# Kernel tuning notes

Measured on AMD Instinct MI355X. Metric: run time of the kernel, lower is better.

The kernel has to match this reference:

```python
import jax, jax.numpy as jnp
import numpy as np

D_K = 64
MASK_FILL = -1e9


def setup_inputs() -> dict:
    key = jax.random.key(0)
    kq, kk, kv, km = jax.random.split(key, 4)
    B, H, S, D = 2, 16, 2048, D_K
    q = jax.random.normal(kq, (B, H, S, D), dtype=jnp.float32)
    k = jax.random.normal(kk, (B, H, D, S), dtype=jnp.float32)  # pre-transposed keys
    v = jax.random.normal(kv, (B, H, S, D), dtype=jnp.float32)
    mask = jax.random.randint(km, (B, H, S, S), 0, 2).astype(jnp.bool_)
    return {"q": q, "k": k, "v": v, "mask": mask}


def reference(q, k, v, mask):
    # scores: [B, H, S, S] = q @ k (k already [B,H,D,S])
    scores = jnp.einsum("bhsd,bhdt->bhst", q, k) / jnp.sqrt(jnp.float32(D_K))
    scores = jnp.where(mask, MASK_FILL, scores)
    attn = jax.nn.softmax(scores, axis=-1)
    context = jnp.einsum("bhst,bhtd->bhsd", attn, v)
    return (context, attn)
```

## Files before the change

kernel.cpp:

```cpp
#include <hip/hip_runtime.h>

#define S_LEN    2048
#define DK       64
#define N_BH     32
#define ROWS     16
#define NTHREADS 512
#define ELDSW    2048

typedef float          f32x4  __attribute__((ext_vector_type(4)));
typedef int            i32x4  __attribute__((ext_vector_type(4)));
typedef short          bf16x8 __attribute__((ext_vector_type(8)));
typedef unsigned short u16x8  __attribute__((ext_vector_type(8)));

__device__ __forceinline__ unsigned short f2bf(float f) {
    unsigned u = __builtin_bit_cast(unsigned, f);
    u += 0x7fffu + ((u >> 16) & 1u);
    return (unsigned short)(u >> 16);
}
__device__ __forceinline__ float bf2f(unsigned short h) {
    unsigned u = ((unsigned)h) << 16;
    return __builtin_bit_cast(float, u);
}

__global__ void prep_qcast(const float* __restrict__ q, unsigned short* __restrict__ Qb) {
    const long i = ((long)blockIdx.x * 256 + threadIdx.x) * 8;
    f32x4 a = *(const f32x4*)(q + i);
    f32x4 b = *(const f32x4*)(q + i + 4);
    u16x8 o;
    o[0]=f2bf(a.x); o[1]=f2bf(a.y); o[2]=f2bf(a.z); o[3]=f2bf(a.w);
    o[4]=f2bf(b.x); o[5]=f2bf(b.y); o[6]=f2bf(b.z); o[7]=f2bf(b.w);
    *(u16x8*)(Qb + i) = o;
}

__global__ void prep_k(const float* __restrict__ k, unsigned short* __restrict__ Kb) {
    __shared__ float t[64][65];
    const int bh = blockIdx.x >> 5, s0 = (blockIdx.x & 31) << 6;
    const int tx = threadIdx.x;
    const float* kb = k + (long)bh * 64 * S_LEN;
    #pragma unroll
    for (int i = 0; i < 16; ++i) {
        const int d = (i << 2) + (tx >> 6), s = tx & 63;
        t[d][s] = kb[(long)d * S_LEN + s0 + s];
    }
    __syncthreads();
    #pragma unroll
    for (int i = 0; i < 16; ++i) {
        const int s = (i << 2) + (tx >> 6), d = tx & 63;
        Kb[((long)bh * S_LEN + s0 + s) * DK + d] = f2bf(t[d][s]);
    }
}

__global__ void prep_v(const float* __restrict__ v, unsigned short* __restrict__ Vb) {
    __shared__ float t[64][65];
    const int bh = blockIdx.x >> 5, s0 = (blockIdx.x & 31) << 6;
    const int tx = threadIdx.x;
    #pragma unroll
    for (int i = 0; i < 16; ++i) {
        const int s = (i << 2) + (tx >> 6), d = tx & 63;
        t[s][d] = v[((long)bh * S_LEN + s0 + s) * DK + d];
    }
    __syncthreads();
    #pragma unroll
    for (int i = 0; i < 16; ++i) {
        const int d = (i << 2) + (tx >> 6), s = tx & 63;
        Vb[((long)bh * DK + d) * S_LEN + s0 + s] = f2bf(t[s][d]);
    }
}

template <bool WS>
__global__ __launch_bounds__(NTHREADS, 4)
void sdpa_main(const float* __restrict__ q, const float* __restrict__ k,
               const float* __restrict__ v, const int* __restrict__ mask,
               const unsigned short* __restrict__ Qb,
               const unsigned short* __restrict__ Kb,
               const unsigned short* __restrict__ Vb,
               float* __restrict__ ctx, float* __restrict__ attn)
{
    extern __shared__ unsigned short elds[];
    __shared__ float ctxlds[ROWS * DK];
    __shared__ float invlds[ROWS];

    const int bid  = blockIdx.x;
    const int bh   = bid & (N_BH - 1);
    const int qt   = bid >> 5;
    const int tid  = threadIdx.x;
    const int wave = tid >> 6;
    const int lane = tid & 63;
    const int m    = lane & 15;
    const int g    = lane >> 4;
    const long rowbase = (long)bh * S_LEN + qt * ROWS;

    for (int i = tid; i < ROWS * DK; i += NTHREADS) ctxlds[i] = 0.0f;

    {
        bf16x8 afrag[2];
        if (WS) {
            const unsigned short* qp = Qb + (rowbase + m) * DK;
            afrag[0] = *(const bf16x8*)(qp + g * 8);
            afrag[1] = *(const bf16x8*)(qp + 32 + g * 8);
        } else {
            const float* qp = q + (rowbase + m) * DK;
            #pragma unroll
            for (int ks = 0; ks < 2; ++ks) {
                const float* p = qp + ks * 32 + g * 8;
                f32x4 x0 = *(const f32x4*)p, x1 = *(const f32x4*)(p + 4);
                afrag[ks][0]=(short)f2bf(x0.x); afrag[ks][1]=(short)f2bf(x0.y);
                afrag[ks][2]=(short)f2bf(x0.z); afrag[ks][3]=(short)f2bf(x0.w);
                afrag[ks][4]=(short)f2bf(x1.x); afrag[ks][5]=(short)f2bf(x1.y);
                afrag[ks][6]=(short)f2bf(x1.z); afrag[ks][7]=(short)f2bf(x1.w);
            }
        }
        const int qcol = wave << 8;
        for (int ct = 0; ct < 16; ++ct) {
            const int t0 = qcol + (ct << 4);
            const int tc = t0 + m;
            f32x4 acc = {0.f, 0.f, 0.f, 0.f};
            #pragma unroll
            for (int ks = 0; ks < 2; ++ks) {
                bf16x8 bfrag;
                if (WS) {
                    bfrag = *(const bf16x8*)(Kb + ((long)bh * S_LEN + tc) * DK + ks * 32 + g * 8);
                } else {
                    const float* kp = k + (long)bh * DK * S_LEN + (long)(ks * 32 + g * 8) * S_LEN + tc;
                    #pragma unroll
                    for (int j = 0; j < 8; ++j) bfrag[j] = (short)f2bf(kp[(long)j * S_LEN]);
                }
                acc = __builtin_amdgcn_mfma_f32_16x16x32_bf16(afrag[ks], bfrag, acc, 0, 0, 0);
            }
            #pragma unroll
            for (int i = 0; i < 4; ++i) {
                const int row = 4 * g + i;
                const float e = __expf(acc[i] * 0.125f);
                elds[row * ELDSW + (tc ^ ((row & 7) << 3))] = f2bf(e);
            }
        }
    }
    __syncthreads();

    {
        const int r   = tid >> 5;
        const int j32 = tid & 31;
        unsigned short* erow = elds + r * ELDSW;
        const int sw8 = (r & 7) << 3;
        const long arow = (rowbase + r) * (long)S_LEN;
        const int* mrow = mask + arow;
        float rsum = 0.f;
        #pragma unroll
        for (int i = 0; i < 8; ++i) {
            const int t  = (j32 << 3) + (i << 8);
            const int ts = t ^ sw8;
            u16x8 ev = *(u16x8*)(erow + ts);
            i32x4 m0 = __builtin_nontemporal_load((const i32x4*)(mrow + t));
            i32x4 m1 = __builtin_nontemporal_load((const i32x4*)(mrow + t + 4));
            if (m0.x) ev[0] = 0;  if (m0.y) ev[1] = 0;
            if (m0.z) ev[2] = 0;  if (m0.w) ev[3] = 0;
            if (m1.x) ev[4] = 0;  if (m1.y) ev[5] = 0;
            if (m1.z) ev[6] = 0;  if (m1.w) ev[7] = 0;
            *(u16x8*)(erow + ts) = ev;
            rsum += ((bf2f(ev[0]) + bf2f(ev[1])) + (bf2f(ev[2]) + bf2f(ev[3])))
                  + ((bf2f(ev[4]) + bf2f(ev[5])) + (bf2f(ev[6]) + bf2f(ev[7])));
        }
        #pragma unroll
        for (int off = 16; off; off >>= 1) rsum += __shfl_xor(rsum, off);
        const float rinv = 1.0f / rsum;
        if (j32 == 0) invlds[r] = rinv;
        float* aout = attn + arow;
        #pragma unroll
        for (int i = 0; i < 8; ++i) {
            const int t  = (j32 << 3) + (i << 8);
            const int ts = t ^ sw8;
            u16x8 ev = *(u16x8*)(erow + ts);
            f32x4 o0 = { bf2f(ev[0]) * rinv, bf2f(ev[1]) * rinv,
                         bf2f(ev[2]) * rinv, bf2f(ev[3]) * rinv };
            f32x4 o1 = { bf2f(ev[4]) * rinv, bf2f(ev[5]) * rinv,
                         bf2f(ev[6]) * rinv, bf2f(ev[7]) * rinv };
            __builtin_nontemporal_store(o0, (f32x4*)(aout + t));
            __builtin_nontemporal_store(o1, (f32x4*)(aout + t + 4));
        }
    }
    __syncthreads();

    {
        const int d0 = (wave & 3) << 4;
        const int kh = wave >> 2;
        const int swm = (m & 7) << 3;
        f32x4 cacc = {0.f, 0.f, 0.f, 0.f};
        for (int ks = 0; ks < 32; ++ks) {
            const int cb = (kh << 10) + (ks << 5) + (g << 3);
            bf16x8 af = *(const bf16x8*)(elds + m * ELDSW + (cb ^ swm));
            bf16x8 bfv;
            if (WS) {
                bfv = *(const bf16x8*)(Vb + ((long)bh * DK + d0 + m) * S_LEN + (kh << 10) + (ks << 5) + g * 8);
            } else {
                const float* vp = v + (long)bh * S_LEN * DK + (long)((kh << 10) + (ks << 5) + g * 8) * DK + d0 + m;
                #pragma unroll
                for (int j = 0; j < 8; ++j) bfv[j] = (short)f2bf(vp[j * DK]);
            }
            cacc = __builtin_amdgcn_mfma_f32_16x16x32_bf16(af, bfv, cacc, 0, 0, 0);
        }
        #pragma unroll
        for (int i = 0; i < 4; ++i)
            atomicAdd(&ctxlds[(4 * g + i) * DK + d0 + m], cacc[i]);
    }
    __syncthreads();

    for (int i = tid; i < ROWS * DK; i += NTHREADS) {
        const int rr = i >> 6, dd = i & 63;
        ctx[(rowbase + rr) * DK + dd] = ctxlds[i] * invlds[rr];
    }
}

extern "C" void kernel_launch(void* const* d_in, const int* in_sizes, int n_in,
                              void* d_out, int out_size, void* d_ws, size_t ws_size,
                              hipStream_t stream)
{
    const float* q    = (const float*)d_in[0];
    const float* k    = (const float*)d_in[1];
    const float* v    = (const float*)d_in[2];
    const int*   mask = (const int*)d_in[3];

    float* ctx  = (float*)d_out;
    float* attn = ctx + (size_t)N_BH * S_LEN * DK;

    const size_t nel = (size_t)N_BH * S_LEN * DK;
    const bool use_ws = ws_size >= nel * 3 * sizeof(unsigned short);
    unsigned short* Qb = (unsigned short*)d_ws;
    unsigned short* Kb = Qb + nel;
    unsigned short* Vb = Kb + nel;

    const size_t shbytes = (size_t)ROWS * ELDSW * sizeof(unsigned short);
    const int nblocks = N_BH * (S_LEN / ROWS);

    if (use_ws) {
        prep_qcast<<<(int)(nel / (256 * 8)), 256, 0, stream>>>(q, Qb);
        prep_k<<<N_BH * (S_LEN / 64), 256, 0, stream>>>(k, Kb);
        prep_v<<<N_BH * (S_LEN / 64), 256, 0, stream>>>(v, Vb);
        (void)hipFuncSetAttribute((const void*)sdpa_main<true>,
                                  hipFuncAttributeMaxDynamicSharedMemorySize, (int)shbytes);
        sdpa_main<true><<<nblocks, NTHREADS, shbytes, stream>>>(q, k, v, mask, Qb, Kb, Vb, ctx, attn);
    } else {
        (void)hipFuncSetAttribute((const void*)sdpa_main<false>,
                                  hipFuncAttributeMaxDynamicSharedMemorySize, (int)shbytes);
        sdpa_main<false><<<nblocks, NTHREADS, shbytes, stream>>>(q, k, v, mask,
                                                                 nullptr, nullptr, nullptr, ctx, attn);
    }
}
```

Baseline: 413.5 us.

## Halve query rows per block to 8 and swap MFMA operand roles

Reduces each block from 16 to 8 query rows, halving the LDS score buffer so more blocks can be resident per CU. The launch-bounds occupancy hint rises from 4 to 8. The QK MFMA now takes K as the A operand and Q as B, so each lane writes four contiguous columns and only the lanes holding valid rows (m<8) store. The softmax pass now assigns one wave per row, and in the PV stage only the valid half of the accumulator is added into LDS. The cost is that half of every MFMA computes padded rows, and K and V are re-read from memory twice as often per query row.

Result: slower. 618.8 us (+49.7%).

```diff
diff --git a/kernel.cpp b/kernel.cpp
--- a/kernel.cpp
+++ b/kernel.cpp
@@ -3,14 +3,14 @@
 #define S_LEN    2048
 #define DK       64
 #define N_BH     32
-#define ROWS     16
+#define ROWS     8
 #define NTHREADS 512
-#define ELDSW    2048
 
 typedef float          f32x4  __attribute__((ext_vector_type(4)));
 typedef int            i32x4  __attribute__((ext_vector_type(4)));
 typedef short          bf16x8 __attribute__((ext_vector_type(8)));
 typedef unsigned short u16x8  __attribute__((ext_vector_type(8)));
+typedef unsigned short u16x4  __attribute__((ext_vector_type(4)));
 
 __device__ __forceinline__ unsigned short f2bf(float f) {
     unsigned u = __builtin_bit_cast(unsigned, f);
@@ -68,7 +68,7 @@
 }
 
 template <bool WS>
-__global__ __launch_bounds__(NTHREADS, 4)
+__global__ __launch_bounds__(NTHREADS, 8)
 void sdpa_main(const float* __restrict__ q, const float* __restrict__ k,
                const float* __restrict__ v, const int* __restrict__ mask,
                const unsigned short* __restrict__ Qb,
@@ -88,67 +88,70 @@
     const int lane = tid & 63;
     const int m    = lane & 15;
     const int g    = lane >> 4;
+    const int mr   = m & 7;
     const long rowbase = (long)bh * S_LEN + qt * ROWS;
 
-    for (int i = tid; i < ROWS * DK; i += NTHREADS) ctxlds[i] = 0.0f;
-
-    {
-        bf16x8 afrag[2];
+    ctxlds[tid] = 0.0f;
+
+    {
+        bf16x8 qfrag[2];
         if (WS) {
-            const unsigned short* qp = Qb + (rowbase + m) * DK;
-            afrag[0] = *(const bf16x8*)(qp + g * 8);
-            afrag[1] = *(const bf16x8*)(qp + 32 + g * 8);
+            const unsigned short* qp = Qb + (rowbase + mr) * DK;
+            qfrag[0] = *(const bf16x8*)(qp + g * 8);
+            qfrag[1] = *(const bf16x8*)(qp + 32 + g * 8);
         } else {
-            const float* qp = q + (rowbase + m) * DK;
+            const float* qp = q + (rowbase + mr) * DK;
             #pragma unroll
             for (int ks = 0; ks < 2; ++ks) {
                 const float* p = qp + ks * 32 + g * 8;
                 f32x4 x0 = *(const f32x4*)p, x1 = *(const f32x4*)(p + 4);
-                afrag[ks][0]=(short)f2bf(x0.x); afrag[ks][1]=(short)f2bf(x0.y);
-                afrag[ks][2]=(short)f2bf(x0.z); afrag[ks][3]=(short)f2bf(x0.w);
-                afrag[ks][4]=(short)f2bf(x1.x); afrag[ks][5]=(short)f2bf(x1.y);
-                afrag[ks][6]=(short)f2bf(x1.z); afrag[ks][7]=(short)f2bf(x1.w);
-            }
-        }
-        const int qcol = wave << 8;
+                qfrag[ks][0]=(short)f2bf(x0.x); qfrag[ks][1]=(short)f2bf(x0.y);
+                qfrag[ks][2]=(short)f2bf(x0.z); qfrag[ks][3]=(short)f2bf(x0.w);
+                qfrag[ks][4]=(short)f2bf(x1.x); qfrag[ks][5]=(short)f2bf(x1.y);
+                qfrag[ks][6]=(short)f2bf(x1.z); qfrag[ks][7]=(short)f2bf(x1.w);
+            }
+        }
         for (int ct = 0; ct < 16; ++ct) {
-            const int t0 = qcol + (ct << 4);
-            const int tc = t0 + m;
+            const int t0 = (wave << 8) + (ct << 4);
+            const int tk = t0 + m;
             f32x4 acc = {0.f, 0.f, 0.f, 0.f};
             #pragma unroll
             for (int ks = 0; ks < 2; ++ks) {
-                bf16x8 bfrag;
+                bf16x8 kfrag;
                 if (WS) {
-                    bfrag = *(const bf16x8*)(Kb + ((long)bh * S_LEN + tc) * DK + ks * 32 + g * 8);
+                    kfrag = *(const bf16x8*)(Kb + ((long)bh * S_LEN + tk) * DK + ks * 32 + g * 8);
                 } else {
-                    const float* kp = k + (long)bh * DK * S_LEN + (long)(ks * 32 + g * 8) * S_LEN + tc;
+                    const float* kp = k + (long)bh * DK * S_LEN + (long)(ks * 32 + g * 8) * S_LEN + tk;
                     #pragma unroll
-                    for (int j = 0; j < 8; ++j) bfrag[j] = (short)f2bf(kp[(long)j * S_LEN]);
+                    for (int j = 0; j < 8; ++j) kfrag[j] = (short)f2bf(kp[(long)j * S_LEN]);
                 }
-                acc = __builtin_amdgcn_mfma_f32_16x16x32_bf16(afrag[ks], bfrag, acc, 0, 0, 0);
-            }
-            #pragma unroll
-            for (int i = 0; i < 4; ++i) {
-                const int row = 4 * g + i;
-                const float e = __expf(acc[i] * 0.125f);
-                elds[row * ELDSW + (tc ^ ((row & 7) << 3))] = f2bf(e);
-            }
-        }
-    }
-    __syncthreads();
-
-    {
-        const int r   = tid >> 5;
-        const int j32 = tid & 31;
-        unsigned short* erow = elds + r * ELDSW;
-        const int sw8 = (r & 7) << 3;
+                acc = __builtin_amdgcn_mfma_f32_16x16x32_bf16(kfrag, qfrag[ks], acc, 0, 0, 0);
+            }
+            if (m < 8) {
+                u16x4 w;
+                w[0] = f2bf(__expf(acc[0] * 0.125f));
+                w[1] = f2bf(__expf(acc[1] * 0.125f));
+                w[2] = f2bf(__expf(acc[2] * 0.125f));
+                w[3] = f2bf(__expf(acc[3] * 0.125f));
+                const int col = (t0 + (g << 2)) ^ (m << 3);
+                *(u16x4*)(elds + m * 2048 + col) = w;
+            }
+        }
+    }
+    __syncthreads();
+
+    {
+        const int r = wave;
+        const int j = lane;
+        unsigned short* erow = elds + r * 2048;
+        const int sw = r << 3;
         const long arow = (rowbase + r) * (long)S_LEN;
         const int* mrow = mask + arow;
         float rsum = 0.f;
         #pragma unroll
-        for (int i = 0; i < 8; ++i) {
-            const int t  = (j32 << 3) + (i << 8);
-            const int ts = t ^ sw8;
+        for (int i = 0; i < 4; ++i) {
+            const int t  = (j << 3) + (i << 9);
+            const int ts = t ^ sw;
             u16x8 ev = *(u16x8*)(erow + ts);
             i32x4 m0 = __builtin_nontemporal_load((const i32x4*)(mrow + t));
             i32x4 m1 = __builtin_nontemporal_load((const i32x4*)(mrow + t + 4));
@@ -161,14 +164,14 @@
                   + ((bf2f(ev[4]) + bf2f(ev[5])) + (bf2f(ev[6]) + bf2f(ev[7])));
         }
         #pragma unroll
-        for (int off = 16; off; off >>= 1) rsum += __shfl_xor(rsum, off);
+        for (int off = 32; off; off >>= 1) rsum += __shfl_xor(rsum, off);
         const float rinv = 1.0f / rsum;
-        if (j32 == 0) invlds[r] = rinv;
+        if (j == 0) invlds[r] = rinv;
         float* aout = attn + arow;
         #pragma unroll
-        for (int i = 0; i < 8; ++i) {
-            const int t  = (j32 << 3) + (i << 8);
-            const int ts = t ^ sw8;
+        for (int i = 0; i < 4; ++i) {
+            const int t  = (j << 3) + (i << 9);
+            const int ts = t ^ sw;
             u16x8 ev = *(u16x8*)(erow + ts);
             f32x4 o0 = { bf2f(ev[0]) * rinv, bf2f(ev[1]) * rinv,
                          bf2f(ev[2]) * rinv, bf2f(ev[3]) * rinv };
@@ -183,30 +186,33 @@
     {
         const int d0 = (wave & 3) << 4;
         const int kh = wave >> 2;
-        const int swm = (m & 7) << 3;
+        const int sw = mr << 3;
+        const unsigned short* arow = elds + mr * 2048;
         f32x4 cacc = {0.f, 0.f, 0.f, 0.f};
         for (int ks = 0; ks < 32; ++ks) {
             const int cb = (kh << 10) + (ks << 5) + (g << 3);
-            bf16x8 af = *(const bf16x8*)(elds + m * ELDSW + (cb ^ swm));
+            bf16x8 af = *(const bf16x8*)(arow + (cb ^ sw));
             bf16x8 bfv;
             if (WS) {
-                bfv = *(const bf16x8*)(Vb + ((long)bh * DK + d0 + m) * S_LEN + (kh << 10) + (ks << 5) + g * 8);
+                bfv = *(const bf16x8*)(Vb + ((long)bh * DK + d0 + m) * S_LEN + cb);
             } else {
-                const float* vp = v + (long)bh * S_LEN * DK + (long)((kh << 10) + (ks << 5) + g * 8) * DK + d0 + m;
+                const float* vp = v + (long)bh * S_LEN * DK + (long)cb * DK + d0 + m;
                 #pragma unroll
                 for (int j = 0; j < 8; ++j) bfv[j] = (short)f2bf(vp[j * DK]);
             }
             cacc = __builtin_amdgcn_mfma_f32_16x16x32_bf16(af, bfv, cacc, 0, 0, 0);
         }
-        #pragma unroll
-        for (int i = 0; i < 4; ++i)
-            atomicAdd(&ctxlds[(4 * g + i) * DK + d0 + m], cacc[i]);
-    }
-    __syncthreads();
-
-    for (int i = tid; i < ROWS * DK; i += NTHREADS) {
-        const int rr = i >> 6, dd = i & 63;
-        ctx[(rowbase + rr) * DK + dd] = ctxlds[i] * invlds[rr];
+        if (g < 2) {
+            #pragma unroll
+            for (int i = 0; i < 4; ++i)
+                atomicAdd(&ctxlds[(4 * g + i) * DK + d0 + m], cacc[i]);
+        }
+    }
+    __syncthreads();
+
+    {
+        const int rr = tid >> 6, dd = tid & 63;
+        ctx[(rowbase + rr) * DK + dd] = ctxlds[tid] * invlds[rr];
     }
 }
 
@@ -228,7 +234,7 @@
     unsigned short* Kb = Qb + nel;
     unsigned short* Vb = Kb + nel;
 
-    const size_t shbytes = (size_t)ROWS * ELDSW * sizeof(unsigned short);
+    const size_t shbytes = (size_t)ROWS * 2048 * sizeof(unsigned short);
     const int nblocks = N_BH * (S_LEN / ROWS);
 
     if (use_ws) {
```
